# Optimization experiments

Measured on AMD Instinct MI355X. Metric: run time of the kernel, lower is better.

## Reference

```python
import jax, jax.numpy as jnp
import numpy as np

N = 102400   # total nodes
F = 400      # node features
E = 1638400  # edges
H = 64       # hidden channels
L = 3        # num_layers (hidden convs); +1 final conv to width 1
K = 300      # sort-pool k
NPER = 400   # nodes per graph (uniform graphs)
B = N // NPER
D = H * L + 1  # total_latent_dim = 193


def setup_inputs() -> dict:
    key = jax.random.key(0)
    ks = jax.random.split(key, 20)
    def lin(k, i, o):
        return jax.random.normal(k, (i, o), jnp.float32) / np.sqrt(i)
    inp = {
        "x": jax.random.normal(ks[0], (N, F), jnp.float32),
        "edge_index": jax.random.randint(ks[1], (2, E), 0, N, jnp.int64),
        "W1": lin(ks[2], F, H), "b1": jnp.zeros((H,), jnp.float32),
        "W2": lin(ks[3], H, H), "b2": jnp.zeros((H,), jnp.float32),
        "W3": lin(ks[4], H, H), "b3": jnp.zeros((H,), jnp.float32),
        "W4": lin(ks[5], H, 1), "b4": jnp.zeros((1,), jnp.float32),
        "cw1": jax.random.normal(ks[6], (16, 1, D), jnp.float32) / np.sqrt(D),
        "cb1": jnp.zeros((16,), jnp.float32),
        "cw2": jax.random.normal(ks[7], (32, 16, 5), jnp.float32) / np.sqrt(16 * 5),
        "cb2": jnp.zeros((32,), jnp.float32),
        "mw1": lin(ks[8], 4672, 32), "mb1": jnp.zeros((32,), jnp.float32),
        "mw2": lin(ks[9], 32, 2), "mb2": jnp.zeros((2,), jnp.float32),
    }
    return inp


def _gcn(x, W, b, src, dst, norm):
    h = x @ W                                   # [N, out]
    msg = h[src] * norm[:, None]                # [E', out]
    out = jax.ops.segment_sum(msg, dst, num_segments=N)
    return out + b


def reference(x, edge_index, W1, b1, W2, b2, W3, b3, W4, b4,
              cw1, cb1, cw2, cb2, mw1, mb1, mw2, mb2):
    # GCN normalization with self-loops (D^-1/2 (A+I) D^-1/2)
    loops = jnp.arange(N, dtype=edge_index.dtype)
    src = jnp.concatenate([edge_index[0], loops])
    dst = jnp.concatenate([edge_index[1], loops])
    deg = jax.ops.segment_sum(jnp.ones_like(src, jnp.float32), dst, num_segments=N)
    dis = jax.lax.rsqrt(jnp.maximum(deg, 1.0))
    norm = dis[src] * dis[dst]

    h1 = jnp.tanh(_gcn(x, W1, b1, src, dst, norm))
    h2 = jnp.tanh(_gcn(h1, W2, b2, src, dst, norm))
    h3 = jnp.tanh(_gcn(h2, W3, b3, src, dst, norm))
    h4 = jnp.tanh(_gcn(h3, W4, b4, src, dst, norm))
    feat = jnp.concatenate([h1, h2, h3, h4], axis=-1)  # [N, D]

    # SortAggregation: per-graph sort by last channel (descending), take top-k
    fg = feat.reshape(B, NPER, D)
    order = jnp.argsort(-fg[:, :, -1], axis=1)[:, :K]  # [B, K]
    pooled = jnp.take_along_axis(fg, order[:, :, None], axis=1)  # [B, K, D]
    z = pooled.reshape(B, 1, K * D)

    dn = ("NCH", "OIH", "NCH")
    z = jax.lax.conv_general_dilated(z, cw1, (D,), "VALID", dimension_numbers=dn)
    z = jax.nn.relu(z + cb1[None, :, None])            # [B, 16, K]
    z = jax.lax.reduce_window(z, -jnp.inf, jax.lax.max, (1, 1, 2), (1, 1, 2), "VALID")
    z = jax.lax.conv_general_dilated(z, cw2, (1,), "VALID", dimension_numbers=dn)
    z = jax.nn.relu(z + cb2[None, :, None])            # [B, 32, 146]
    z = z.reshape(B, -1)                               # [B, 4672]
    z = jax.nn.relu(z @ mw1 + mb1)
    return z @ mw2 + mb2                               # [B, 2]
```

## Files before the change

### kernel.cpp

```cpp
#include <hip/hip_runtime.h>
#include <cstdint>
#include <cstddef>

#define Nn 102400
#define Ff 400
#define Ee 1638400
#define Kk 300
#define Bb 256
#define CAP 64

__device__ __forceinline__ float xla_tanhf(float x) {
    const float c = 7.90531110763549805f;
    float xc = fminf(fmaxf(x, -c), c);
    float x2 = __fmul_rn(xc, xc);
    float p = -2.76076847742355e-16f;
    p = __fadd_rn(__fmul_rn(p, x2),  2.00018790482477e-13f);
    p = __fadd_rn(__fmul_rn(p, x2), -8.60467152213735e-11f);
    p = __fadd_rn(__fmul_rn(p, x2),  5.12229709037114e-08f);
    p = __fadd_rn(__fmul_rn(p, x2),  1.48572235717979e-05f);
    p = __fadd_rn(__fmul_rn(p, x2),  6.37261928875436e-04f);
    p = __fadd_rn(__fmul_rn(p, x2),  4.89352455891786e-03f);
    p = __fmul_rn(p, xc);
    float q = 1.19825839466702e-06f;
    q = __fadd_rn(__fmul_rn(q, x2), 1.18534705686654e-04f);
    q = __fadd_rn(__fmul_rn(q, x2), 2.26843463243900e-03f);
    q = __fadd_rn(__fmul_rn(q, x2), 4.89352518554385e-03f);
    float r = __fdiv_rn(p, q);
    return (fabsf(x) < 0.0004f) ? x : r;
}

template <int CH>
__device__ __forceinline__ void gemm_wave(const float* __restrict__ A,
                                          const float* __restrict__ B,
                                          float* __restrict__ C,
                                          int tile, int tid,
                                          float* __restrict__ Asw,
                                          float* __restrict__ Bsw) {
    constexpr int K = 16 * CH;
    int tx = tid & 15;
    int ty = tid >> 4;
    int base = tile * 32;
    int sr = tid >> 1, sh = tid & 1;
    int bk = tid >> 2, bn = (tid & 3) * 16;
    const float* aip = A + (size_t)(base + sr) * K + sh * 8;
    const float* bip = B + (size_t)bk * 64 + bn;
    float acc[8][4] = {};
    float4 aA0, aA1, aB0, aB1;
    float4 bA[4], bB[4];
    auto LOADG = [&](int ch, float4& a0, float4& a1, float4 (&bv)[4]) {
        const float* ap = aip + ch * 16;
        a0 = *(const float4*)(ap);
        a1 = *(const float4*)(ap + 4);
        const float* bp = bip + (size_t)ch * 16 * 64;
        bv[0] = *(const float4*)(bp);
        bv[1] = *(const float4*)(bp + 4);
        bv[2] = *(const float4*)(bp + 8);
        bv[3] = *(const float4*)(bp + 12);
    };
    auto STORE = [&](const float4& a0, const float4& a1, const float4 (&bv)[4]) {
        Asw[(sh * 8 + 0) * 32 + sr] = a0.x;
        Asw[(sh * 8 + 1) * 32 + sr] = a0.y;
        Asw[(sh * 8 + 2) * 32 + sr] = a0.z;
        Asw[(sh * 8 + 3) * 32 + sr] = a0.w;
        Asw[(sh * 8 + 4) * 32 + sr] = a1.x;
        Asw[(sh * 8 + 5) * 32 + sr] = a1.y;
        Asw[(sh * 8 + 6) * 32 + sr] = a1.z;
        Asw[(sh * 8 + 7) * 32 + sr] = a1.w;
        *(float4*)&Bsw[bk * 68 + bn]      = bv[0];
        *(float4*)&Bsw[bk * 68 + bn + 4]  = bv[1];
        *(float4*)&Bsw[bk * 68 + bn + 8]  = bv[2];
        *(float4*)&Bsw[bk * 68 + bn + 12] = bv[3];
    };
    auto COMPUTE = [&]() {
#pragma unroll
        for (int kk = 0; kk < 16; ++kk) {
            float4 f0 = *(const float4*)&Asw[kk * 32 + ty * 8];
            float4 f1 = *(const float4*)&Asw[kk * 32 + ty * 8 + 4];
            float2 b01 = *(const float2*)&Bsw[kk * 68 + tx * 2];
            float2 b23 = *(const float2*)&Bsw[kk * 68 + 32 + tx * 2];
            float av[8] = {f0.x, f0.y, f0.z, f0.w, f1.x, f1.y, f1.z, f1.w};
            float bv2[4] = {b01.x, b01.y, b23.x, b23.y};
#pragma unroll
            for (int r = 0; r < 8; ++r)
#pragma unroll
                for (int c = 0; c < 4; ++c) acc[r][c] = fmaf(av[r], bv2[c], acc[r][c]);
        }
    };
    LOADG(0, aA0, aA1, bA);
    int ch = 0;
    while (true) {
        STORE(aA0, aA1, bA);
        if (ch + 1 < CH) LOADG(ch + 1, aB0, aB1, bB);
        COMPUTE();
        if (++ch >= CH) break;
        STORE(aB0, aB1, bB);
        if (ch + 1 < CH) LOADG(ch + 1, aA0, aA1, bA);
        COMPUTE();
        if (++ch >= CH) break;
    }
#pragma unroll
    for (int r = 0; r < 8; ++r) {
        float* cp = C + (size_t)(base + ty * 8 + r) * 64;
        *(float2*)(cp + tx * 2)      = make_float2(acc[r][0], acc[r][1]);
        *(float2*)(cp + 32 + tx * 2) = make_float2(acc[r][2], acc[r][3]);
    }
}

template <int CH>
__global__ __launch_bounds__(256) void gemm_k(const float* __restrict__ A,
                                              const float* __restrict__ B,
                                              float* __restrict__ C) {
    __shared__ __align__(16) float As[4][16 * 32];
    __shared__ __align__(16) float Bs[4][16 * 68];
    int wid = threadIdx.x >> 6, tid = threadIdx.x & 63;
    gemm_wave<CH>(A, B, C, blockIdx.x * 4 + wid, tid, As[wid], Bs[wid]);
}

__global__ __launch_bounds__(256) void fat_k(const int* __restrict__ ei,
                                             int* __restrict__ fill,
                                             int* __restrict__ csr,
                                             const float* __restrict__ x,
                                             const float* __restrict__ W1,
                                             float* __restrict__ t) {
    __shared__ __align__(16) float As[4][16 * 32];
    __shared__ __align__(16) float Bs[4][16 * 68];
    int b = blockIdx.x;
    int g = b / 9, r = b - g * 9;
    if (r == 0) {
        int wid = threadIdx.x >> 6, tid = threadIdx.x & 63;
        gemm_wave<25>(x, W1, t, g * 4 + wid, tid, As[wid], Bs[wid]);
    } else {
        int e = (g * 8 + (r - 1)) * 256 + threadIdx.x;
        int d = ei[Ee + e];
        int p = atomicAdd(&fill[(size_t)d * 16], 1);
        if (p < CAP) csr[(size_t)d * CAP + p] = e;
    }
}

__global__ __launch_bounds__(256) void sortrow_k(const int* __restrict__ ei,
                                                 const int* __restrict__ fill,
                                                 int* __restrict__ csr,
                                                 float* __restrict__ dis,
                                                 int* __restrict__ degc) {
    int lane = threadIdx.x & 63;
    int v = blockIdx.x * 4 + (threadIdx.x >> 6);
    int dvf = fill[(size_t)v * 16];
    int dv = min(dvf, CAP);
    if (lane == 0) { dis[v] = 1.0f / sqrtf((float)(dvf + 1)); degc[v] = dvf; }
    int key = (lane < dv) ? csr[(size_t)v * CAP + lane] : 0x7FFFFFFF;
#pragma unroll
    for (int k = 2; k <= 64; k <<= 1) {
#pragma unroll
        for (int j = k >> 1; j; j >>= 1) {
            int other = __shfl_xor(key, j);
            bool up = ((lane & k) == 0);
            bool lower = ((lane & j) == 0);
            key = (lower == up) ? min(key, other) : max(key, other);
        }
    }
    if (lane < dv) csr[(size_t)v * CAP + lane] = ei[key];
}

template <int PHASE>
__global__ __launch_bounds__(256, 4) void agg64_k(const float* __restrict__ t,
                                                  const float* __restrict__ bias,
                                                  const float* __restrict__ dis,
                                                  const int* __restrict__ degc,
                                                  const int* __restrict__ csr,
                                                  float* __restrict__ nrm,
                                                  float* __restrict__ out,
                                                  const float* __restrict__ W4,
                                                  float* __restrict__ t4) {
    int lane = threadIdx.x & 63;
    int wv = __builtin_amdgcn_readfirstlane(threadIdx.x >> 6);
    int v = blockIdx.x * 4 + wv;
    int dv = __builtin_amdgcn_readfirstlane(min(degc[v], CAP));
    float dsv = dis[v];
    float tself = t[(size_t)v * 64 + lane];
    float bsl = bias[lane];
    int idxl = (lane < dv) ? csr[(size_t)v * CAP + lane] : v;
    float nr;
    if (PHASE == 1) {
        nr = __fmul_rn(dis[idxl], dsv);
        nrm[(size_t)v * 64 + lane] = nr;
    } else {
        nr = nrm[(size_t)v * 64 + lane];
    }
    float acc = 0.0f;
    int j = 0;
    for (; j + 16 <= dv; j += 16) {
        float tv[16];
#pragma unroll
        for (int q = 0; q < 16; ++q) {
            int u = __builtin_amdgcn_readfirstlane(__shfl(idxl, j + q));
            tv[q] = t[(size_t)u * 64 + lane];
        }
#pragma unroll
        for (int q = 0; q < 16; ++q)
            acc = __fadd_rn(acc, __fmul_rn(tv[q], __shfl(nr, j + q)));
    }
    for (; j + 4 <= dv; j += 4) {
        float tv[4];
#pragma unroll
        for (int q = 0; q < 4; ++q) {
            int u = __builtin_amdgcn_readfirstlane(__shfl(idxl, j + q));
            tv[q] = t[(size_t)u * 64 + lane];
        }
#pragma unroll
        for (int q = 0; q < 4; ++q)
            acc = __fadd_rn(acc, __fmul_rn(tv[q], __shfl(nr, j + q)));
    }
    for (; j < dv; ++j) {
        int u = __builtin_amdgcn_readfirstlane(__shfl(idxl, j));
        acc = __fadd_rn(acc, __fmul_rn(t[(size_t)u * 64 + lane], __shfl(nr, j)));
    }
    acc = __fadd_rn(acc, __fmul_rn(tself, __fmul_rn(dsv, dsv)));
    float res = xla_tanhf(__fadd_rn(acc, bsl));
    out[(size_t)v * 64 + lane] = res;
    if (W4 != nullptr) {
        float w4l = W4[lane];
        float a4 = 0.0f;
#pragma unroll
        for (int k = 0; k < 64; ++k) {
            float hk = __shfl(res, k);
            float wk = __shfl(w4l, k);
            a4 = fmaf(hk, wk, a4);
        }
        if (lane == 0) t4[v] = a4;
    }
}

__global__ void agg1_k(const float* __restrict__ t4, const float* __restrict__ dis,
                       const int* __restrict__ degc, const int* __restrict__ csr,
                       const float* __restrict__ nrm,
                       const float* __restrict__ b4, float* __restrict__ h4) {
    int v = blockIdx.x * 256 + threadIdx.x;
    if (v >= Nn) return;
    int dv = min(degc[v], CAP);
    float dsv = dis[v];
    const int* row = csr + (size_t)v * CAP;
    const float* nr = nrm + (size_t)v * 64;
    float acc = 0.0f;
    int j = 0;
    for (; j + 16 <= dv; j += 16) {
        int u[16]; float nv[16], tv[16];
#pragma unroll
        for (int q = 0; q < 16; ++q) nv[q] = nr[j + q];
#pragma unroll
        for (int q = 0; q < 16; ++q) u[q] = row[j + q];
#pragma unroll
        for (int q = 0; q < 16; ++q) tv[q] = t4[u[q]];
#pragma unroll
        for (int q = 0; q < 16; ++q)
            acc = __fadd_rn(acc, __fmul_rn(tv[q], nv[q]));
    }
    for (; j + 4 <= dv; j += 4) {
        int u[4]; float nv[4], tv[4];
#pragma unroll
        for (int q = 0; q < 4; ++q) nv[q] = nr[j + q];
#pragma unroll
        for (int q = 0; q < 4; ++q) u[q] = row[j + q];
#pragma unroll
        for (int q = 0; q < 4; ++q) tv[q] = t4[u[q]];
#pragma unroll
        for (int q = 0; q < 4; ++q)
            acc = __fadd_rn(acc, __fmul_rn(tv[q], nv[q]));
    }
    for (; j < dv; ++j)
        acc = __fadd_rn(acc, __fmul_rn(t4[row[j]], nr[j]));
    acc = __fadd_rn(acc, __fmul_rn(t4[v], __fmul_rn(dsv, dsv)));
    h4[v] = xla_tanhf(__fadd_rn(acc, b4[0]));
}

__global__ __launch_bounds__(512) void sort_k(const float* __restrict__ h4,
                                              int* __restrict__ order) {
    __shared__ unsigned int kv[512];
    __shared__ int ki[512];
    int tid = threadIdx.x, g = blockIdx.x;
    unsigned int key = 0xFFFFFFFFu;
    if (tid < 400) {
        unsigned int u = __float_as_uint(h4[g * 400 + tid]);
        u = (u & 0x80000000u) ? ~u : (u | 0x80000000u);
        key = ~u;
    }
    kv[tid] = key; ki[tid] = tid;
    __syncthreads();
    for (int size = 2; size <= 512; size <<= 1) {
        for (int stride = size >> 1; stride > 0; stride >>= 1) {
            int p = tid ^ stride;
            if (p > tid) {
                bool asc = ((tid & size) == 0);
                unsigned int a = kv[tid], b = kv[p];
                int ia = ki[tid], ib = ki[p];
                bool gt = (a > b) || (a == b && ia > ib);
                if (gt == asc) { kv[tid] = b; kv[p] = a; ki[tid] = ib; ki[p] = ia; }
            }
            __syncthreads();
        }
    }
    if (tid < Kk) order[g * Kk + tid] = ki[tid];
}

__global__ __launch_bounds__(128) void conv1_k(const float* __restrict__ h1,
                                               const float* __restrict__ h2,
                                               const float* __restrict__ h3,
                                               const float* __restrict__ h4,
                                               const int* __restrict__ order,
                                               const float* __restrict__ cw1,
                                               const float* __restrict__ cb1,
                                               float* __restrict__ z1) {
    __shared__ double wt[193 * 16];
    int tid = threadIdx.x, b = blockIdx.y;
    for (int i = tid; i < 193 * 16; i += 128) {
        int c = i / 193, d = i % 193;
        wt[d * 16 + c] = (double)cw1[i];
    }
    __syncthreads();
    int kpos = blockIdx.x * 128 + tid;
    if (kpos >= Kk) return;
    int n = b * 400 + order[b * Kk + kpos];
    double acc[16];
#pragma unroll
    for (int c = 0; c < 16; ++c) acc[c] = (double)cb1[c];
    const float* bases[3] = {h1 + (size_t)n * 64, h2 + (size_t)n * 64, h3 + (size_t)n * 64};
    for (int r = 0; r < 3; ++r) {
        const float* p = bases[r];
        for (int d = 0; d < 64; ++d) {
            double xv = (double)p[d];
            const double* wp = &wt[((size_t)r * 64 + d) * 16];
#pragma unroll
            for (int c = 0; c < 16; ++c) acc[c] += xv * wp[c];
        }
    }
    double xl = (double)h4[n];
    {
        const double* wp = &wt[192 * 16];
#pragma unroll
        for (int c = 0; c < 16; ++c) acc[c] += xl * wp[c];
    }
#pragma unroll
    for (int c = 0; c < 16; ++c)
        z1[((size_t)b * 16 + c) * 300 + kpos] = (float)fmax(acc[c], 0.0);
}

__global__ __launch_bounds__(256) void tail_k(const float* __restrict__ z1,
                                              const float* __restrict__ cw2,
                                              const float* __restrict__ cb2,
                                              const float* __restrict__ mw1,
                                              const float* __restrict__ mb1,
                                              const float* __restrict__ mw2,
                                              const float* __restrict__ mb2,
                                              float* __restrict__ out) {
    __shared__ float lz[16 * 150];
    __shared__ float lw[2560];
    __shared__ float lz3[4672];
    __shared__ double red[256];
    __shared__ double s4[32];
    int b = blockIdx.x, tid = threadIdx.x;
    for (int i = tid; i < 2400; i += 256) {
        int bc = i / 150, j = i % 150;
        const float* zp = z1 + ((size_t)b * 16 + bc) * 300 + 2 * j;
        lz[i] = fmaxf(zp[0], zp[1]);
    }
    for (int i = tid; i < 2560; i += 256) lw[i] = cw2[i];
    __syncthreads();
    for (int o = tid; o < 4672; o += 256) {
        int co = o / 146, j = o % 146;
        float acc = cb2[co];
#pragma unroll
        for (int ci = 0; ci < 16; ++ci)
#pragma unroll
            for (int tt = 0; tt < 5; ++tt)
                acc += lz[ci * 150 + j + tt] * lw[co * 80 + ci * 5 + tt];
        lz3[o] = fmaxf(acc, 0.f);
    }
    __syncthreads();
    int o = tid & 31, part = tid >> 5;
    double acc = 0.0;
    for (int i = part * 584; i < (part + 1) * 584; ++i)
        acc += (double)lz3[i] * (double)mw1[(size_t)i * 32 + o];
    red[tid] = acc;
    __syncthreads();
    if (tid < 32) {
        double s = 0.0;
#pragma unroll
        for (int p = 0; p < 8; ++p) s += red[p * 32 + tid];
        s4[tid] = fmax(s + (double)mb1[tid], 0.0);
    }
    __syncthreads();
    if (tid < 2) {
        double s = (double)mb2[tid];
#pragma unroll
        for (int j = 0; j < 32; ++j) s += s4[j] * (double)mw2[j * 2 + tid];
        out[b * 2 + tid] = (float)s;
    }
}

extern "C" void kernel_launch(void* const* d_in, const int* in_sizes, int n_in,
                              void* d_out, int out_size, void* d_ws, size_t ws_size,
                              hipStream_t stream) {
    const float* x   = (const float*)d_in[0];
    const int*   ei  = (const int*)d_in[1];
    const float* W1  = (const float*)d_in[2];  const float* b1  = (const float*)d_in[3];
    const float* W2  = (const float*)d_in[4];  const float* b2  = (const float*)d_in[5];
    const float* W3  = (const float*)d_in[6];  const float* b3  = (const float*)d_in[7];
    const float* W4  = (const float*)d_in[8];  const float* b4  = (const float*)d_in[9];
    const float* cw1 = (const float*)d_in[10]; const float* cb1 = (const float*)d_in[11];
    const float* cw2 = (const float*)d_in[12]; const float* cb2 = (const float*)d_in[13];
    const float* mw1 = (const float*)d_in[14]; const float* mb1 = (const float*)d_in[15];
    const float* mw2 = (const float*)d_in[16]; const float* mb2 = (const float*)d_in[17];
    float* out = (float*)d_out;

    const size_t N64 = (size_t)Nn * 64;
    float* t    = (float*)d_ws;
    float* h1   = t + N64;
    float* h2   = h1 + N64;
    float* h3   = h2 + N64;
    float* t4   = h3 + N64;
    float* h4   = t4 + Nn;
    float* dis  = h4 + Nn;
    int*   degc = (int*)(dis + Nn);
    int*   fill = degc + Nn;
    int*   csr  = fill + (size_t)Nn * 16;
    float* nrm  = (float*)(csr + (size_t)Nn * CAP);
    int*   order = (int*)(nrm + N64);
    float* z1 = (float*)t;

    hipMemsetAsync(fill, 0, sizeof(int) * (size_t)Nn * 16, stream);

    fat_k<<<7200, 256, 0, stream>>>(ei, fill, csr, x, W1, t);
    sortrow_k<<<Nn / 4, 256, 0, stream>>>(ei, fill, csr, dis, degc);

    agg64_k<1><<<Nn / 4, 256, 0, stream>>>(t, b1, dis, degc, csr, nrm, h1, nullptr, nullptr);
    gemm_k<4><<<Nn / 32 / 4, 256, 0, stream>>>(h1, W2, t);
    agg64_k<0><<<Nn / 4, 256, 0, stream>>>(t, b2, dis, degc, csr, nrm, h2, nullptr, nullptr);
    gemm_k<4><<<Nn / 32 / 4, 256, 0, stream>>>(h2, W3, t);
    agg64_k<0><<<Nn / 4, 256, 0, stream>>>(t, b3, dis, degc, csr, nrm, h3, W4, t4);

    agg1_k<<<Nn / 256, 256, 0, stream>>>(t4, dis, degc, csr, nrm, b4, h4);

    sort_k<<<Bb, 512, 0, stream>>>(h4, order);
    conv1_k<<<dim3(3, Bb), 128, 0, stream>>>(h1, h2, h3, h4, order, cw1, cb1, z1);
    tail_k<<<Bb, 256, 0, stream>>>(z1, cw2, cb2, mw1, mb1, mw2, mb2, out);
}
```

Baseline: 1.115 ms.

## Unfuse edge scatter from first GEMM, shrink GEMM tiles, pad aggregation loop

The fused kernel that did the edge scatter and the x@W1 GEMM in one launch is split in two. The scatter becomes its own kernel that handles two edges per thread, and all GEMMs now use 16-row wave tiles instead of 32 to get more blocks. The aggregation kernel stages neighbor indices and norms in shared memory and pads the neighbor loop to multiples of 32, with padded lanes using zero norm and the self index. This removes the tail loops but adds wasted gathers for low-degree nodes, and the smaller tiles reuse B less per tile.

New measurement: 1.171 ms. 5.0% more time.

```diff
diff --git a/kernel.cpp b/kernel.cpp
--- a/kernel.cpp
+++ b/kernel.cpp
@@ -29,112 +29,15 @@
     return (fabsf(x) < 0.0004f) ? x : r;
 }
 
-template <int CH>
-__device__ __forceinline__ void gemm_wave(const float* __restrict__ A,
-                                          const float* __restrict__ B,
-                                          float* __restrict__ C,
-                                          int tile, int tid,
-                                          float* __restrict__ Asw,
-                                          float* __restrict__ Bsw) {
-    constexpr int K = 16 * CH;
-    int tx = tid & 15;
-    int ty = tid >> 4;
-    int base = tile * 32;
-    int sr = tid >> 1, sh = tid & 1;
-    int bk = tid >> 2, bn = (tid & 3) * 16;
-    const float* aip = A + (size_t)(base + sr) * K + sh * 8;
-    const float* bip = B + (size_t)bk * 64 + bn;
-    float acc[8][4] = {};
-    float4 aA0, aA1, aB0, aB1;
-    float4 bA[4], bB[4];
-    auto LOADG = [&](int ch, float4& a0, float4& a1, float4 (&bv)[4]) {
-        const float* ap = aip + ch * 16;
-        a0 = *(const float4*)(ap);
-        a1 = *(const float4*)(ap + 4);
-        const float* bp = bip + (size_t)ch * 16 * 64;
-        bv[0] = *(const float4*)(bp);
-        bv[1] = *(const float4*)(bp + 4);
-        bv[2] = *(const float4*)(bp + 8);
-        bv[3] = *(const float4*)(bp + 12);
-    };
-    auto STORE = [&](const float4& a0, const float4& a1, const float4 (&bv)[4]) {
-        Asw[(sh * 8 + 0) * 32 + sr] = a0.x;
-        Asw[(sh * 8 + 1) * 32 + sr] = a0.y;
-        Asw[(sh * 8 + 2) * 32 + sr] = a0.z;
-        Asw[(sh * 8 + 3) * 32 + sr] = a0.w;
-        Asw[(sh * 8 + 4) * 32 + sr] = a1.x;
-        Asw[(sh * 8 + 5) * 32 + sr] = a1.y;
-        Asw[(sh * 8 + 6) * 32 + sr] = a1.z;
-        Asw[(sh * 8 + 7) * 32 + sr] = a1.w;
-        *(float4*)&Bsw[bk * 68 + bn]      = bv[0];
-        *(float4*)&Bsw[bk * 68 + bn + 4]  = bv[1];
-        *(float4*)&Bsw[bk * 68 + bn + 8]  = bv[2];
-        *(float4*)&Bsw[bk * 68 + bn + 12] = bv[3];
-    };
-    auto COMPUTE = [&]() {
-#pragma unroll
-        for (int kk = 0; kk < 16; ++kk) {
-            float4 f0 = *(const float4*)&Asw[kk * 32 + ty * 8];
-            float4 f1 = *(const float4*)&Asw[kk * 32 + ty * 8 + 4];
-            float2 b01 = *(const float2*)&Bsw[kk * 68 + tx * 2];
-            float2 b23 = *(const float2*)&Bsw[kk * 68 + 32 + tx * 2];
-            float av[8] = {f0.x, f0.y, f0.z, f0.w, f1.x, f1.y, f1.z, f1.w};
-            float bv2[4] = {b01.x, b01.y, b23.x, b23.y};
-#pragma unroll
-            for (int r = 0; r < 8; ++r)
-#pragma unroll
-                for (int c = 0; c < 4; ++c) acc[r][c] = fmaf(av[r], bv2[c], acc[r][c]);
-        }
-    };
-    LOADG(0, aA0, aA1, bA);
-    int ch = 0;
-    while (true) {
-        STORE(aA0, aA1, bA);
-        if (ch + 1 < CH) LOADG(ch + 1, aB0, aB1, bB);
-        COMPUTE();
-        if (++ch >= CH) break;
-        STORE(aB0, aB1, bB);
-        if (ch + 1 < CH) LOADG(ch + 1, aA0, aA1, bA);
-        COMPUTE();
-        if (++ch >= CH) break;
-    }
-#pragma unroll
-    for (int r = 0; r < 8; ++r) {
-        float* cp = C + (size_t)(base + ty * 8 + r) * 64;
-        *(float2*)(cp + tx * 2)      = make_float2(acc[r][0], acc[r][1]);
-        *(float2*)(cp + 32 + tx * 2) = make_float2(acc[r][2], acc[r][3]);
-    }
-}
-
-template <int CH>
-__global__ __launch_bounds__(256) void gemm_k(const float* __restrict__ A,
-                                              const float* __restrict__ B,
-                                              float* __restrict__ C) {
-    __shared__ __align__(16) float As[4][16 * 32];
-    __shared__ __align__(16) float Bs[4][16 * 68];
-    int wid = threadIdx.x >> 6, tid = threadIdx.x & 63;
-    gemm_wave<CH>(A, B, C, blockIdx.x * 4 + wid, tid, As[wid], Bs[wid]);
-}
-
-__global__ __launch_bounds__(256) void fat_k(const int* __restrict__ ei,
-                                             int* __restrict__ fill,
-                                             int* __restrict__ csr,
-                                             const float* __restrict__ x,
-                                             const float* __restrict__ W1,
-                                             float* __restrict__ t) {
-    __shared__ __align__(16) float As[4][16 * 32];
-    __shared__ __align__(16) float Bs[4][16 * 68];
-    int b = blockIdx.x;
-    int g = b / 9, r = b - g * 9;
-    if (r == 0) {
-        int wid = threadIdx.x >> 6, tid = threadIdx.x & 63;
-        gemm_wave<25>(x, W1, t, g * 4 + wid, tid, As[wid], Bs[wid]);
-    } else {
-        int e = (g * 8 + (r - 1)) * 256 + threadIdx.x;
-        int d = ei[Ee + e];
-        int p = atomicAdd(&fill[(size_t)d * 16], 1);
-        if (p < CAP) csr[(size_t)d * CAP + p] = e;
-    }
+__global__ void scat_k(const int* __restrict__ ei, int* __restrict__ fill,
+                       int* __restrict__ csr) {
+    int g = blockIdx.x * 256 + threadIdx.x;
+    int2 d2 = *(const int2*)(ei + Ee + 2 * g);
+    int e0 = 2 * g, e1 = 2 * g + 1;
+    int p0 = atomicAdd(&fill[(size_t)d2.x * 16], 1);
+    int p1 = atomicAdd(&fill[(size_t)d2.y * 16], 1);
+    if (p0 < CAP) csr[(size_t)d2.x * CAP + p0] = e0;
+    if (p1 < CAP) csr[(size_t)d2.y * CAP + p1] = e1;
 }
 
 __global__ __launch_bounds__(256) void sortrow_k(const int* __restrict__ ei,
@@ -161,6 +64,79 @@
     if (lane < dv) csr[(size_t)v * CAP + lane] = ei[key];
 }
 
+template <int CH>
+__global__ __launch_bounds__(256) void gemm_k(const float* __restrict__ A,
+                                              const float* __restrict__ B,
+                                              float* __restrict__ C) {
+    constexpr int K = 16 * CH;
+    __shared__ __align__(16) float As[4][16 * 16];
+    __shared__ __align__(16) float Bs[4][16 * 68];
+    int wid = threadIdx.x >> 6, tid = threadIdx.x & 63;
+    float* Asw = As[wid];
+    float* Bsw = Bs[wid];
+    int tile = blockIdx.x * 4 + wid;
+    int base = tile * 16;
+    int tx = tid & 15;
+    int ty = tid >> 4;
+    int sr = tid >> 2, sq = tid & 3;
+    int bk = tid >> 2, bn = (tid & 3) * 16;
+    const float* aip = A + (size_t)(base + sr) * K + sq * 4;
+    const float* bip = B + (size_t)bk * 64 + bn;
+    float acc[4][4] = {};
+    float4 aA, aB;
+    float4 bA[4], bB[4];
+    auto LOADG = [&](int ch, float4& a0, float4 (&bv)[4]) {
+        a0 = *(const float4*)(aip + ch * 16);
+        const float* bp = bip + (size_t)ch * 16 * 64;
+        bv[0] = *(const float4*)(bp);
+        bv[1] = *(const float4*)(bp + 4);
+        bv[2] = *(const float4*)(bp + 8);
+        bv[3] = *(const float4*)(bp + 12);
+    };
+    auto STORE = [&](const float4& a0, const float4 (&bv)[4]) {
+        Asw[(sq * 4 + 0) * 16 + sr] = a0.x;
+        Asw[(sq * 4 + 1) * 16 + sr] = a0.y;
+        Asw[(sq * 4 + 2) * 16 + sr] = a0.z;
+        Asw[(sq * 4 + 3) * 16 + sr] = a0.w;
+        *(float4*)&Bsw[bk * 68 + bn]      = bv[0];
+        *(float4*)&Bsw[bk * 68 + bn + 4]  = bv[1];
+        *(float4*)&Bsw[bk * 68 + bn + 8]  = bv[2];
+        *(float4*)&Bsw[bk * 68 + bn + 12] = bv[3];
+    };
+    auto COMPUTE = [&]() {
+#pragma unroll
+        for (int kk = 0; kk < 16; ++kk) {
+            float4 f0 = *(const float4*)&Asw[kk * 16 + ty * 4];
+            float2 b01 = *(const float2*)&Bsw[kk * 68 + tx * 2];
+            float2 b23 = *(const float2*)&Bsw[kk * 68 + 32 + tx * 2];
+            float av[4] = {f0.x, f0.y, f0.z, f0.w};
+            float bv2[4] = {b01.x, b01.y, b23.x, b23.y};
+#pragma unroll
+            for (int r = 0; r < 4; ++r)
+#pragma unroll
+                for (int c = 0; c < 4; ++c) acc[r][c] = fmaf(av[r], bv2[c], acc[r][c]);
+        }
+    };
+    LOADG(0, aA, bA);
+    int ch = 0;
+    while (true) {
+        STORE(aA, bA);
+        if (ch + 1 < CH) LOADG(ch + 1, aB, bB);
+        COMPUTE();
+        if (++ch >= CH) break;
+        STORE(aB, bB);
+        if (ch + 1 < CH) LOADG(ch + 1, aA, bA);
+        COMPUTE();
+        if (++ch >= CH) break;
+    }
+#pragma unroll
+    for (int r = 0; r < 4; ++r) {
+        float* cp = C + (size_t)(base + ty * 4 + r) * 64;
+        *(float2*)(cp + tx * 2)      = make_float2(acc[r][0], acc[r][1]);
+        *(float2*)(cp + 32 + tx * 2) = make_float2(acc[r][2], acc[r][3]);
+    }
+}
+
 template <int PHASE>
 __global__ __launch_bounds__(256, 4) void agg64_k(const float* __restrict__ t,
                                                   const float* __restrict__ bias,
@@ -171,6 +147,8 @@
                                                   float* __restrict__ out,
                                                   const float* __restrict__ W4,
                                                   float* __restrict__ t4) {
+    __shared__ int   sidx[4][64];
+    __shared__ float snr[4][64];
     int lane = threadIdx.x & 63;
     int wv = __builtin_amdgcn_readfirstlane(threadIdx.x >> 6);
     int v = blockIdx.x * 4 + wv;
@@ -181,38 +159,27 @@
     int idxl = (lane < dv) ? csr[(size_t)v * CAP + lane] : v;
     float nr;
     if (PHASE == 1) {
-        nr = __fmul_rn(dis[idxl], dsv);
+        nr = (lane < dv) ? __fmul_rn(dis[idxl], dsv) : 0.0f;
         nrm[(size_t)v * 64 + lane] = nr;
     } else {
         nr = nrm[(size_t)v * 64 + lane];
     }
+    sidx[wv][lane] = idxl;
+    snr[wv][lane] = nr;
+    int dvp = (dv + 31) & ~31;
     float acc = 0.0f;
-    int j = 0;
-    for (; j + 16 <= dv; j += 16) {
-        float tv[16];
-#pragma unroll
-        for (int q = 0; q < 16; ++q) {
-            int u = __builtin_amdgcn_readfirstlane(__shfl(idxl, j + q));
+    for (int j = 0; j < dvp; j += 32) {
+        float tv[32], nv[32];
+#pragma unroll
+        for (int q = 0; q < 32; ++q) {
+            int u = __builtin_amdgcn_readfirstlane(sidx[wv][j + q]);
             tv[q] = t[(size_t)u * 64 + lane];
         }
 #pragma unroll
-        for (int q = 0; q < 16; ++q)
-            acc = __fadd_rn(acc, __fmul_rn(tv[q], __shfl(nr, j + q)));
-    }
-    for (; j + 4 <= dv; j += 4) {
-        float tv[4];
-#pragma unroll
-        for (int q = 0; q < 4; ++q) {
-            int u = __builtin_amdgcn_readfirstlane(__shfl(idxl, j + q));
-            tv[q] = t[(size_t)u * 64 + lane];
-        }
-#pragma unroll
-        for (int q = 0; q < 4; ++q)
-            acc = __fadd_rn(acc, __fmul_rn(tv[q], __shfl(nr, j + q)));
-    }
-    for (; j < dv; ++j) {
-        int u = __builtin_amdgcn_readfirstlane(__shfl(idxl, j));
-        acc = __fadd_rn(acc, __fmul_rn(t[(size_t)u * 64 + lane], __shfl(nr, j)));
+        for (int q = 0; q < 32; ++q) nv[q] = snr[wv][j + q];
+#pragma unroll
+        for (int q = 0; q < 32; ++q)
+            acc = __fadd_rn(acc, __fmul_rn(tv[q], nv[q]));
     }
     acc = __fadd_rn(acc, __fmul_rn(tself, __fmul_rn(dsv, dsv)));
     float res = xla_tanhf(__fadd_rn(acc, bsl));
@@ -428,13 +395,14 @@
 
     hipMemsetAsync(fill, 0, sizeof(int) * (size_t)Nn * 16, stream);
 
-    fat_k<<<7200, 256, 0, stream>>>(ei, fill, csr, x, W1, t);
+    scat_k<<<Ee / 512, 256, 0, stream>>>(ei, fill, csr);
     sortrow_k<<<Nn / 4, 256, 0, stream>>>(ei, fill, csr, dis, degc);
 
+    gemm_k<25><<<Nn / 16 / 4, 256, 0, stream>>>(x, W1, t);
     agg64_k<1><<<Nn / 4, 256, 0, stream>>>(t, b1, dis, degc, csr, nrm, h1, nullptr, nullptr);
-    gemm_k<4><<<Nn / 32 / 4, 256, 0, stream>>>(h1, W2, t);
+    gemm_k<4> <<<Nn / 16 / 4, 256, 0, stream>>>(h1, W2, t);
     agg64_k<0><<<Nn / 4, 256, 0, stream>>>(t, b2, dis, degc, csr, nrm, h2, nullptr, nullptr);
-    gemm_k<4><<<Nn / 32 / 4, 256, 0, stream>>>(h2, W3, t);
+    gemm_k<4> <<<Nn / 16 / 4, 256, 0, stream>>>(h2, W3, t);
     agg64_k<0><<<Nn / 4, 256, 0, stream>>>(t, b3, dis, degc, csr, nrm, h3, W4, t4);
 
     agg1_k<<<Nn / 256, 256, 0, stream>>>(t4, dis, degc, csr, nrm, b4, h4);
```
